# Optimization experiments

Measured on AMD Instinct MI355X. Metric: run time of the kernel, lower is better.

The kernel has to match this reference:

```python
import jax, jax.numpy as jnp
import numpy as np

NUM_VIDEOS = 1024       # B
SECTIONS_PER_VIDEO = 32 # avg segment length (uniform here for simplicity)
NUM_CLASSES = 1024      # C
TOTAL_SECTIONS = NUM_VIDEOS * SECTIONS_PER_VIDEO
EPS = 1e-4


def setup_inputs() -> dict:
    key = jax.random.key(0)
    k1, k2, k3 = jax.random.split(key, 3)
    # scores are probabilities (module uses BCELoss directly on them)
    section_scores = jax.random.uniform(k1, (TOTAL_SECTIONS, NUM_CLASSES),
                                        minval=EPS, maxval=1.0 - EPS, dtype=jnp.float32)
    video_scores = jax.random.uniform(k2, (NUM_VIDEOS, NUM_CLASSES),
                                      minval=EPS, maxval=1.0 - EPS, dtype=jnp.float32)
    labels = (jax.random.uniform(k3, (NUM_VIDEOS, NUM_CLASSES)) > 0.5).astype(jnp.float32)
    # flat encoding of the ragged `segments` list: section i belongs to video segment_ids[i]
    segment_ids = jnp.repeat(jnp.arange(NUM_VIDEOS, dtype=jnp.int32), SECTIONS_PER_VIDEO)
    return {"section_scores": section_scores, "video_scores": video_scores,
            "labels": labels, "segment_ids": segment_ids}


def _bce(p, y):
    # torch.nn.BCELoss(reduction='mean'): mean over all elements
    return -jnp.mean(y * jnp.log(p) + (1.0 - y) * jnp.log1p(-p))


def reference(section_scores, video_scores, labels, segment_ids):
    # fused ragged per-video max-reduce over sections (replaces the Python loop)
    video_scores_from_sections = jax.ops.segment_max(
        section_scores, segment_ids, num_segments=NUM_VIDEOS)  # [B, C]
    video_loss = _bce(video_scores, labels)
    video_loss_from_sections = _bce(video_scores_from_sections, labels)
    return video_loss + video_loss_from_sections
```

## Files before the change

### kernel.cpp

```cpp
#include <hip/hip_runtime.h>


#define NUM_VIDEOS   1024
#define SECS_PER_VID 32
#define NUM_CLASSES  1024

__device__ __forceinline__ float bce_term(float p, float y) {
    float q = (y > 0.5f) ? p : (1.0f - p);
    return -__logf(q) ;
}

__global__ __launch_bounds__(256) void hloss_main_kernel(
    const float* __restrict__ sec,
    const float* __restrict__ vid,
    const float* __restrict__ lab,
    float* __restrict__ partials)
{
    const int v = blockIdx.x;
    const int t = threadIdx.x;

    const float4* secv = reinterpret_cast<const float4*>(sec + (size_t)v * SECS_PER_VID * NUM_CLASSES) + t;
    const float4* vidv = reinterpret_cast<const float4*>(vid + (size_t)v * NUM_CLASSES) + t;
    const float4* labv = reinterpret_cast<const float4*>(lab + (size_t)v * NUM_CLASSES) + t;

    float4 m = secv[0];
    #pragma unroll
    for (int r = 1; r < SECS_PER_VID; ++r) {
        float4 x = secv[r * (NUM_CLASSES / 4)];
        m.x = fmaxf(m.x, x.x);
        m.y = fmaxf(m.y, x.y);
        m.z = fmaxf(m.z, x.z);
        m.w = fmaxf(m.w, x.w);
    }

    float4 p = *vidv;
    float4 y = *labv;

    float s = 0.0f;
    s += bce_term(p.x, y.x) + bce_term(m.x, y.x);
    s += bce_term(p.y, y.y) + bce_term(m.y, y.y);
    s += bce_term(p.z, y.z) + bce_term(m.z, y.z);
    s += bce_term(p.w, y.w) + bce_term(m.w, y.w);

    #pragma unroll
    for (int off = 32; off >= 1; off >>= 1)
        s += __shfl_down(s, off, 64);

    __shared__ float wsum[4];
    const int wave = t >> 6;
    const int lane = t & 63;
    if (lane == 0) wsum[wave] = s;
    __syncthreads();
    if (t == 0)
        partials[v] = wsum[0] + wsum[1] + wsum[2] + wsum[3];
}

__global__ __launch_bounds__(256) void hloss_finalize_kernel(
    const float* __restrict__ partials,
    float* __restrict__ out)
{
    const int t = threadIdx.x;
    double s = 0.0;
    #pragma unroll
    for (int i = 0; i < NUM_VIDEOS / 256; ++i)
        s += (double)partials[t + i * 256];

    #pragma unroll
    for (int off = 32; off >= 1; off >>= 1)
        s += __shfl_down(s, off, 64);

    __shared__ double wsum[4];
    const int wave = t >> 6;
    const int lane = t & 63;
    if (lane == 0) wsum[wave] = s;
    __syncthreads();
    if (t == 0) {
        double total = wsum[0] + wsum[1] + wsum[2] + wsum[3];
        out[0] = (float)(total / (double)((size_t)NUM_VIDEOS * NUM_CLASSES));
    }
}

extern "C" void kernel_launch(void* const* d_in, const int* in_sizes, int n_in,
                              void* d_out, int out_size, void* d_ws, size_t ws_size,
                              hipStream_t stream) {
    const float* sec = (const float*)d_in[0];
    const float* vid = (const float*)d_in[1];
    const float* lab = (const float*)d_in[2];

    float* partials = (float*)d_ws;
    float* out = (float*)d_out;

    hloss_main_kernel<<<NUM_VIDEOS, 256, 0, stream>>>(sec, vid, lab, partials);
    hloss_finalize_kernel<<<1, 256, 0, stream>>>(partials, out);
}
```

Before: 28.06 us.

## Fuse finalize into main kernel via atomicAdd and merge logs into one

```diff
diff --git a/kernel.cpp b/kernel.cpp
--- a/kernel.cpp
+++ b/kernel.cpp
@@ -5,16 +5,11 @@
 #define SECS_PER_VID 32
 #define NUM_CLASSES  1024
 
-__device__ __forceinline__ float bce_term(float p, float y) {
-    float q = (y > 0.5f) ? p : (1.0f - p);
-    return -__logf(q) ;
-}
-
-__global__ __launch_bounds__(256) void hloss_main_kernel(
+__global__ __launch_bounds__(256) void hloss_kernel(
     const float* __restrict__ sec,
     const float* __restrict__ vid,
     const float* __restrict__ lab,
-    float* __restrict__ partials)
+    float* __restrict__ out)
 {
     const int v = blockIdx.x;
     const int t = threadIdx.x;
@@ -36,11 +31,17 @@
     float4 p = *vidv;
     float4 y = *labv;
 
-    float s = 0.0f;
-    s += bce_term(p.x, y.x) + bce_term(m.x, y.x);
-    s += bce_term(p.y, y.y) + bce_term(m.y, y.y);
-    s += bce_term(p.z, y.z) + bce_term(m.z, y.z);
-    s += bce_term(p.w, y.w) + bce_term(m.w, y.w);
+    float qpx = (y.x > 0.5f) ? p.x : (1.0f - p.x);
+    float qpy = (y.y > 0.5f) ? p.y : (1.0f - p.y);
+    float qpz = (y.z > 0.5f) ? p.z : (1.0f - p.z);
+    float qpw = (y.w > 0.5f) ? p.w : (1.0f - p.w);
+    float qmx = (y.x > 0.5f) ? m.x : (1.0f - m.x);
+    float qmy = (y.y > 0.5f) ? m.y : (1.0f - m.y);
+    float qmz = (y.z > 0.5f) ? m.z : (1.0f - m.z);
+    float qmw = (y.w > 0.5f) ? m.w : (1.0f - m.w);
+
+    float prod = ((qpx * qmx) * (qpy * qmy)) * ((qpz * qmz) * (qpw * qmw));
+    float s = -__logf(prod);
 
     #pragma unroll
     for (int off = 32; off >= 1; off >>= 1)
@@ -51,32 +52,9 @@
     const int lane = t & 63;
     if (lane == 0) wsum[wave] = s;
     __syncthreads();
-    if (t == 0)
-        partials[v] = wsum[0] + wsum[1] + wsum[2] + wsum[3];
-}
-
-__global__ __launch_bounds__(256) void hloss_finalize_kernel(
-    const float* __restrict__ partials,
-    float* __restrict__ out)
-{
-    const int t = threadIdx.x;
-    double s = 0.0;
-    #pragma unroll
-    for (int i = 0; i < NUM_VIDEOS / 256; ++i)
-        s += (double)partials[t + i * 256];
-
-    #pragma unroll
-    for (int off = 32; off >= 1; off >>= 1)
-        s += __shfl_down(s, off, 64);
-
-    __shared__ double wsum[4];
-    const int wave = t >> 6;
-    const int lane = t & 63;
-    if (lane == 0) wsum[wave] = s;
-    __syncthreads();
     if (t == 0) {
-        double total = wsum[0] + wsum[1] + wsum[2] + wsum[3];
-        out[0] = (float)(total / (double)((size_t)NUM_VIDEOS * NUM_CLASSES));
+        const float inv = 1.0f / ((float)NUM_VIDEOS * (float)NUM_CLASSES);
+        atomicAdd(out, (wsum[0] + wsum[1] + wsum[2] + wsum[3]) * inv);
     }
 }
 
@@ -87,9 +65,8 @@
     const float* vid = (const float*)d_in[1];
     const float* lab = (const float*)d_in[2];
 
-    float* partials = (float*)d_ws;
     float* out = (float*)d_out;
 
-    hloss_main_kernel<<<NUM_VIDEOS, 256, 0, stream>>>(sec, vid, lab, partials);
-    hloss_finalize_kernel<<<1, 256, 0, stream>>>(partials, out);
+    hipMemsetAsync(out, 0, sizeof(float), stream);
+    hloss_kernel<<<NUM_VIDEOS, 256, 0, stream>>>(sec, vid, lab, out);
 }
```

Result: slower. 34.43 us (+22.7%).

## Split section max across two half-blocks and fuse logs into one product

Applied to the files above, without the earlier changes.

```diff
diff --git a/kernel.cpp b/kernel.cpp
--- a/kernel.cpp
+++ b/kernel.cpp
@@ -5,27 +5,24 @@
 #define SECS_PER_VID 32
 #define NUM_CLASSES  1024
 
-__device__ __forceinline__ float bce_term(float p, float y) {
-    float q = (y > 0.5f) ? p : (1.0f - p);
-    return -__logf(q) ;
-}
-
-__global__ __launch_bounds__(256) void hloss_main_kernel(
+__global__ __launch_bounds__(512, 8) void hloss_main_kernel(
     const float* __restrict__ sec,
     const float* __restrict__ vid,
     const float* __restrict__ lab,
     float* __restrict__ partials)
 {
-    const int v = blockIdx.x;
-    const int t = threadIdx.x;
+    const int v    = blockIdx.x;
+    const int t    = threadIdx.x;
+    const int half = t >> 8;
+    const int tc   = t & 255;
 
-    const float4* secv = reinterpret_cast<const float4*>(sec + (size_t)v * SECS_PER_VID * NUM_CLASSES) + t;
-    const float4* vidv = reinterpret_cast<const float4*>(vid + (size_t)v * NUM_CLASSES) + t;
-    const float4* labv = reinterpret_cast<const float4*>(lab + (size_t)v * NUM_CLASSES) + t;
+    const float4* secv = reinterpret_cast<const float4*>(
+        sec + (size_t)v * SECS_PER_VID * NUM_CLASSES
+            + (size_t)half * 16 * NUM_CLASSES) + tc;
 
     float4 m = secv[0];
     #pragma unroll
-    for (int r = 1; r < SECS_PER_VID; ++r) {
+    for (int r = 1; r < 16; ++r) {
         float4 x = secv[r * (NUM_CLASSES / 4)];
         m.x = fmaxf(m.x, x.x);
         m.y = fmaxf(m.y, x.y);
@@ -33,26 +30,46 @@
         m.w = fmaxf(m.w, x.w);
     }
 
-    float4 p = *vidv;
-    float4 y = *labv;
+    __shared__ float4 mbuf[256];
+    if (half == 1) mbuf[tc] = m;
+    __syncthreads();
 
     float s = 0.0f;
-    s += bce_term(p.x, y.x) + bce_term(m.x, y.x);
-    s += bce_term(p.y, y.y) + bce_term(m.y, y.y);
-    s += bce_term(p.z, y.z) + bce_term(m.z, y.z);
-    s += bce_term(p.w, y.w) + bce_term(m.w, y.w);
+    if (half == 0) {
+        float4 u = mbuf[tc];
+        m.x = fmaxf(m.x, u.x);
+        m.y = fmaxf(m.y, u.y);
+        m.z = fmaxf(m.z, u.z);
+        m.w = fmaxf(m.w, u.w);
+
+        float4 p = reinterpret_cast<const float4*>(vid + (size_t)v * NUM_CLASSES)[tc];
+        float4 y = reinterpret_cast<const float4*>(lab + (size_t)v * NUM_CLASSES)[tc];
+
+        float qpx = (y.x > 0.5f) ? p.x : (1.0f - p.x);
+        float qpy = (y.y > 0.5f) ? p.y : (1.0f - p.y);
+        float qpz = (y.z > 0.5f) ? p.z : (1.0f - p.z);
+        float qpw = (y.w > 0.5f) ? p.w : (1.0f - p.w);
+        float qmx = (y.x > 0.5f) ? m.x : (1.0f - m.x);
+        float qmy = (y.y > 0.5f) ? m.y : (1.0f - m.y);
+        float qmz = (y.z > 0.5f) ? m.z : (1.0f - m.z);
+        float qmw = (y.w > 0.5f) ? m.w : (1.0f - m.w);
+
+        float prod = ((qpx * qmx) * (qpy * qmy)) * ((qpz * qmz) * (qpw * qmw));
+        s = -__logf(prod);
+    }
 
     #pragma unroll
     for (int off = 32; off >= 1; off >>= 1)
         s += __shfl_down(s, off, 64);
 
-    __shared__ float wsum[4];
+    __shared__ float wsum[8];
     const int wave = t >> 6;
     const int lane = t & 63;
     if (lane == 0) wsum[wave] = s;
     __syncthreads();
     if (t == 0)
-        partials[v] = wsum[0] + wsum[1] + wsum[2] + wsum[3];
+        partials[v] = ((wsum[0] + wsum[1]) + (wsum[2] + wsum[3]))
+                    + ((wsum[4] + wsum[5]) + (wsum[6] + wsum[7]));
 }
 
 __global__ __launch_bounds__(256) void hloss_finalize_kernel(
@@ -60,10 +77,8 @@
     float* __restrict__ out)
 {
     const int t = threadIdx.x;
-    double s = 0.0;
-    #pragma unroll
-    for (int i = 0; i < NUM_VIDEOS / 256; ++i)
-        s += (double)partials[t + i * 256];
+    float4 pp = reinterpret_cast<const float4*>(partials)[t];
+    double s = (double)pp.x + (double)pp.y + (double)pp.z + (double)pp.w;
 
     #pragma unroll
     for (int off = 32; off >= 1; off >>= 1)
@@ -90,6 +105,6 @@
     float* partials = (float*)d_ws;
     float* out = (float*)d_out;
 
-    hloss_main_kernel<<<NUM_VIDEOS, 256, 0, stream>>>(sec, vid, lab, partials);
+    hloss_main_kernel<<<NUM_VIDEOS, 512, 0, stream>>>(sec, vid, lab, partials);
     hloss_finalize_kernel<<<1, 256, 0, stream>>>(partials, out);
 }
```

Result: slower. 29.04 us (+3.5%).
